# Performance work log

Measured on AMD Instinct MI355X. Metric: run time of the kernel, lower is better.

The kernel has to match this reference:

```python
import jax, jax.numpy as jnp
import numpy as np

VOCAB = 400000
DIM = 300
NUM_QUERIES = 512
TOP_K = 5


def setup_inputs() -> dict:
    key = jax.random.key(0)
    k1, k2 = jax.random.split(key)
    embedding = jax.random.normal(k1, (VOCAB, DIM), dtype=jnp.float32)
    word_ids = jax.random.randint(k2, (NUM_QUERIES,), 0, VOCAB, dtype=jnp.int64)
    return {"embedding": embedding, "word_ids": word_ids, "k": TOP_K}


def reference(embedding, word_ids, k):
    # Row-normalize the table (done in Synonym.__init__: emb / emb.norm(dim=1, keepdim=True))
    E = embedding / jnp.linalg.norm(embedding, axis=1, keepdims=True)  # [V, d]
    # Per-word GEMV against the full table, batched over queries:
    # torch.mm(word_embedding.view(1,-1), embedding.t()) per word -> [Q, V]
    q = E[word_ids]                      # [Q, d] gather of query word vectors
    sims = jnp.einsum('qd,vd->qv', q, E)  # [Q, V] cosine similarities
    # topk(k, largest=True); the torch code sorts results by value afterwards,
    # lax.top_k already returns values in descending order.
    top_vals, top_ids = jax.lax.top_k(sims, k)  # [Q, k], [Q, k]
    return top_vals, top_ids
```

## Files before the change

kernel.cpp:

```cpp
#include <hip/hip_runtime.h>


#define VOCAB   400000
#define DIM     300
#define NQ      512
#define NT      25000
#define TILE_U  5120
#define QFSTR   304
#define TOPK    5
#define NCAND   3072

using f32x4 = __attribute__((ext_vector_type(4))) float;
using s16x8 = __attribute__((ext_vector_type(8))) short;

__device__ __forceinline__ unsigned short f2bf(float f) {
  unsigned int u = __builtin_bit_cast(unsigned int, f);
  u += 0x7fffu + ((u >> 16) & 1u);
  return (unsigned short)(u >> 16);
}

__device__ __forceinline__ void ins3(float v, int id, float* tv, int* ti) {
  if (v > tv[2]) {
    if (v > tv[0]) {
      tv[2] = tv[1]; ti[2] = ti[1]; tv[1] = tv[0]; ti[1] = ti[0];
      tv[0] = v; ti[0] = id;
    } else if (v > tv[1]) {
      tv[2] = tv[1]; ti[2] = ti[1]; tv[1] = v; ti[1] = id;
    } else {
      tv[2] = v; ti[2] = id;
    }
  }
}

__global__ __launch_bounds__(64)
void qprep_kernel(const float* __restrict__ emb, const int* __restrict__ wid,
                  float* __restrict__ qf, unsigned short* __restrict__ qsw) {
  const int q = blockIdx.x;
  const int lane = threadIdx.x;
  const long long w = (long long)wid[q];
  const float* row = emb + w * DIM;
  float x[5];
  double ss = 0.0;
#pragma unroll
  for (int j = 0; j < 5; ++j) {
    const int k = lane + 64 * j;
    x[j] = (k < DIM) ? row[k] : 0.0f;
    ss += (double)x[j] * (double)x[j];
  }
#pragma unroll
  for (int m = 1; m < 64; m <<= 1) ss += __shfl_xor(ss, m, 64);
  const double rinv = 1.0 / sqrt(ss);
#pragma unroll
  for (int j = 0; j < 5; ++j) {
    const int k = lane + 64 * j;
    if (k < DIM) qf[q * QFSTR + k] = (float)((double)x[j] * rinv);
  }
  if (lane < 40) {
    const int ks = lane >> 2, grp = lane & 3;
    const int k0 = ks * 32 + grp * 8;
    unsigned int pw[4];
#pragma unroll
    for (int h = 0; h < 4; ++h) {
      const int k = k0 + 2 * h;
      float v0 = 0.f, v1 = 0.f;
      if (k < DIM)     v0 = (float)((double)row[k] * rinv);
      if (k + 1 < DIM) v1 = (float)((double)row[k + 1] * rinv);
      pw[h] = (unsigned int)f2bf(v0) | ((unsigned int)f2bf(v1) << 16);
    }
    uint4 pk; pk.x = pw[0]; pk.y = pw[1]; pk.z = pw[2]; pk.w = pw[3];
    *(uint4*)(qsw + (size_t)(q >> 4) * TILE_U + ks * 512 + grp * 128 + (q & 15) * 8) = pk;
  }
}

__global__ __launch_bounds__(256)
void prenorm_kernel(const float* __restrict__ emb, unsigned short* __restrict__ sw) {
  const int wave = threadIdx.x >> 6, lane = threadIdx.x & 63;
  const int t = blockIdx.x * 4 + wave;
  const int r = lane & 15, grp = lane >> 4;
  const float* row = emb + (size_t)(t * 16 + r) * DIM;

  float x[10][8];
  float ss = 0.f;
#pragma unroll
  for (int ks = 0; ks < 10; ++ks) {
    const int k0 = ks * 32 + grp * 8;
    if (k0 + 8 <= DIM) {
      const f32x4 u = *(const f32x4*)(row + k0);
      const f32x4 v = *(const f32x4*)(row + k0 + 4);
#pragma unroll
      for (int j = 0; j < 4; ++j) { x[ks][j] = u[j]; x[ks][j + 4] = v[j]; }
    } else {
#pragma unroll
      for (int j = 0; j < 8; ++j) {
        const int k = k0 + j;
        x[ks][j] = (k < DIM) ? row[k] : 0.0f;
      }
    }
#pragma unroll
    for (int j = 0; j < 8; ++j) ss += x[ks][j] * x[ks][j];
  }
  ss += __shfl_xor(ss, 16, 64);
  ss += __shfl_xor(ss, 32, 64);
  const float rinv = rsqrtf(ss);

  unsigned short* dst = sw + (size_t)t * TILE_U + lane * 8;
#pragma unroll
  for (int ks = 0; ks < 10; ++ks) {
    uint4 pk;
    unsigned int w0 = f2bf(x[ks][0] * rinv) | ((unsigned int)f2bf(x[ks][1] * rinv) << 16);
    unsigned int w1 = f2bf(x[ks][2] * rinv) | ((unsigned int)f2bf(x[ks][3] * rinv) << 16);
    unsigned int w2 = f2bf(x[ks][4] * rinv) | ((unsigned int)f2bf(x[ks][5] * rinv) << 16);
    unsigned int w3 = f2bf(x[ks][6] * rinv) | ((unsigned int)f2bf(x[ks][7] * rinv) << 16);
    pk.x = w0; pk.y = w1; pk.z = w2; pk.w = w3;
    *(uint4*)(dst + ks * 512) = pk;
  }
}

__global__ __launch_bounds__(256, 4)
void score_kernel(const unsigned short* __restrict__ sw,
                  const unsigned short* __restrict__ qsw,
                  float2* __restrict__ cand) {
  __shared__ __align__(16) unsigned short qlds[4 * TILE_U];

  const int tid = threadIdx.x;
  const int wave = tid >> 6, lane = tid & 63;
  const int l15 = lane & 15, grp = lane >> 4;
  const int bid = blockIdx.x;
  const int moct = (bid >> 3) & 7;
  const int rb = (bid & 7) | ((bid >> 6) << 3);

  {
    const uint4* src = (const uint4*)(qsw + (size_t)moct * 4 * TILE_U);
    uint4* dst = (uint4*)qlds;
#pragma unroll
    for (int i = 0; i < 10; ++i) dst[tid + 256 * i] = src[tid + 256 * i];
  }
  __syncthreads();

  float v3[4][3]; int i3[4][3];
#pragma unroll
  for (int qi = 0; qi < 4; ++qi)
#pragma unroll
    for (int j = 0; j < 3; ++j) { v3[qi][j] = -1e30f; i3[qi][j] = 0; }

  const unsigned short* bq = qlds + lane * 8;
  const int wt = rb * 16 + wave * 4;
  const int nit = (wt < 424) ? 13 : 12;

  for (int it = 0; it < nit; ++it) {
    const int t0 = it * 2048 + wt;
    const unsigned short* ap = sw + (size_t)t0 * TILE_U + lane * 8;

    f32x4 acc[4][4];
#pragma unroll
    for (int qi = 0; qi < 4; ++qi)
#pragma unroll
      for (int vi = 0; vi < 4; ++vi) acc[qi][vi] = {0.f, 0.f, 0.f, 0.f};

#pragma unroll
    for (int ks = 0; ks < 10; ++ks) {
      s16x8 a[4];
#pragma unroll
      for (int vi = 0; vi < 4; ++vi)
        a[vi] = *(const s16x8*)(ap + (size_t)vi * TILE_U + ks * 512);
#pragma unroll
      for (int qi = 0; qi < 4; ++qi) {
        const s16x8 b = *(const s16x8*)(bq + qi * TILE_U + ks * 512);
#pragma unroll
        for (int vi = 0; vi < 4; ++vi)
          acc[qi][vi] = __builtin_amdgcn_mfma_f32_16x16x32_bf16(a[vi], b, acc[qi][vi], 0, 0, 0);
      }
    }

#pragma unroll
    for (int vi = 0; vi < 4; ++vi) {
      const int rbase = (t0 + vi) * 16 + grp * 4;
#pragma unroll
      for (int qi = 0; qi < 4; ++qi) {
        const f32x4 a4 = acc[qi][vi];
        const float m01 = fmaxf(a4[0], a4[1]);
        const float m23 = fmaxf(a4[2], a4[3]);
        if (fmaxf(m01, m23) > v3[qi][2]) {
#pragma unroll
          for (int rr = 0; rr < 4; ++rr)
            ins3(a4[rr], rbase + rr, &v3[qi][0], &i3[qi][0]);
        }
      }
    }
  }

#pragma unroll
  for (int qi = 0; qi < 4; ++qi) {
    float m0 = v3[qi][0], m1 = v3[qi][1], m2 = v3[qi][2];
    int   d0 = i3[qi][0], d1 = i3[qi][1], d2 = i3[qi][2];
    const int q = moct * 64 + qi * 16 + l15;
    float2* dst = cand + (size_t)q * NCAND + (rb * 24 + wave * 6);
#pragma unroll
    for (int r = 0; r < 6; ++r) {
      float bv = m0; int bi = d0; int bl = grp;
      float ov = __shfl_xor(bv, 16, 64);
      int   oi = __shfl_xor(bi, 16, 64);
      int   ol = __shfl_xor(bl, 16, 64);
      if (ov > bv || (ov == bv && ol < bl)) { bv = ov; bi = oi; bl = ol; }
      ov = __shfl_xor(bv, 32, 64);
      oi = __shfl_xor(bi, 32, 64);
      ol = __shfl_xor(bl, 32, 64);
      if (ov > bv || (ov == bv && ol < bl)) { bv = ov; bi = oi; bl = ol; }
      if (bl == grp) { m0 = m1; d0 = d1; m1 = m2; d1 = d2; m2 = -1e30f; }
      if (r == grp || r == grp + 4) {
        float2 e; e.x = bv; e.y = __int_as_float(bi);
        dst[r] = e;
      }
    }
  }
}

__global__ __launch_bounds__(256)
void topk_kernel(const float* __restrict__ emb, const float* __restrict__ qf,
                 const float2* __restrict__ cand, float* __restrict__ out) {
  __shared__ float pV[256 * 6];
  __shared__ int   pI[256 * 6];
  __shared__ int   selI[32];
  __shared__ float resV[32];

  const int q = blockIdx.x;
  const int t = threadIdx.x;
  const float2* cq = cand + (size_t)q * NCAND;

  float bv[6]; int bi[6];
#pragma unroll
  for (int j = 0; j < 6; ++j) { bv[j] = -1e30f; bi[j] = -1; }
  for (int i = t; i < NCAND; i += 256) {
    const float2 e = cq[i];
    const float v = e.x;
    if (v > bv[5]) {
      bv[5] = v; bi[5] = __float_as_int(e.y);
#pragma unroll
      for (int j = 5; j > 0; --j) {
        if (bv[j] > bv[j - 1]) {
          const float tv2 = bv[j]; bv[j] = bv[j - 1]; bv[j - 1] = tv2;
          const int ti2 = bi[j]; bi[j] = bi[j - 1]; bi[j - 1] = ti2;
        }
      }
    }
  }
#pragma unroll
  for (int j = 0; j < 6; ++j) { pV[t * 6 + j] = bv[j]; pI[t * 6 + j] = bi[j]; }
  __syncthreads();

  if (t < 64) {
    for (int r = 0; r < 32; ++r) {
      float mv = -2e30f; int mp = 0;
      for (int i = t; i < 256 * 6; i += 64) {
        const float v = pV[i];
        if (v > mv) { mv = v; mp = i; }
      }
#pragma unroll
      for (int m = 1; m < 64; m <<= 1) {
        const float ov = __shfl_xor(mv, m, 64);
        const int   op = __shfl_xor(mp, m, 64);
        if (ov > mv) { mv = ov; mp = op; }
      }
      if (t == 0) { selI[r] = pI[mp]; pV[mp] = -2e30f; }
      __builtin_amdgcn_wave_barrier();
    }
  }
  __syncthreads();

  {
    const int j = t >> 3, sub = t & 7;
    const int id = selI[j];
    float dot = 0.f, sq = 0.f;
    if (id >= 0) {
      const f32x4* e4 = (const f32x4*)(emb + (size_t)id * DIM);
      const f32x4* q4 = (const f32x4*)(qf + (size_t)q * QFSTR);
      for (int f = sub; f < DIM / 4; f += 8) {
        const f32x4 ev = e4[f], qv = q4[f];
        dot += ev[0]*qv[0] + ev[1]*qv[1] + ev[2]*qv[2] + ev[3]*qv[3];
        sq  += ev[0]*ev[0] + ev[1]*ev[1] + ev[2]*ev[2] + ev[3]*ev[3];
      }
    }
#pragma unroll
    for (int m = 1; m < 8; m <<= 1) {
      dot += __shfl_xor(dot, m, 64);
      sq  += __shfl_xor(sq, m, 64);
    }
    if (sub == 0)
      resV[j] = (id >= 0 && sq > 0.f) ? (float)((double)dot / sqrt((double)sq)) : -2e30f;
  }
  __syncthreads();

  if (t == 0) {
#pragma unroll
    for (int r = 0; r < TOPK; ++r) {
      float mv = -3e30f; int mp = 0;
      for (int i = 0; i < 32; ++i) if (resV[i] > mv) { mv = resV[i]; mp = i; }
      out[q * TOPK + r] = mv;
      out[NQ * TOPK + q * TOPK + r] = (float)selI[mp];
      resV[mp] = -3e30f;
    }
  }
}

extern "C" void kernel_launch(void* const* d_in, const int* in_sizes, int n_in,
                              void* d_out, int out_size, void* d_ws, size_t ws_size,
                              hipStream_t stream) {
  (void)in_sizes; (void)n_in; (void)out_size; (void)ws_size;
  const float* emb = (const float*)d_in[0];
  const int* wid = (const int*)d_in[1];
  float* out = (float*)d_out;

  char* ws = (char*)d_ws;
  unsigned short* qsw = (unsigned short*)ws;
  float*  qf   = (float*)(ws + 327680);
  float2* cand = (float2*)(ws + 950272);
  unsigned short* sw = (unsigned short*)(ws + 13533184);

  qprep_kernel<<<NQ, 64, 0, stream>>>(emb, wid, qf, qsw);
  prenorm_kernel<<<NT / 4, 256, 0, stream>>>(emb, sw);
  score_kernel<<<1024, 256, 0, stream>>>(sw, qsw, cand);
  topk_kernel<<<NQ, 256, 0, stream>>>(emb, qf, cand, out);
}
```

Measured before the change: 1.246 ms.

## Restructure score kernel into 512-thread blocks with register double-buffered A loads

The score kernel now uses 512-thread blocks that each hold 128 queries in LDS. Each wave handles 2 vocab tiles by 64 queries rather than 4 by 64, and the next k-slice of the table is prefetched into registers (double-buffered) so global loads overlap the MFMAs. The prenorm kernel stages 64 rows into LDS with coalesced vector loads before normalizing, replacing the strided per-row reads. Together these aim to hide memory latency and cut uncoalesced traffic, at the cost of more LDS per block, which may lower occupancy.

```diff
diff --git a/kernel.cpp b/kernel.cpp
--- a/kernel.cpp
+++ b/kernel.cpp
@@ -74,10 +74,25 @@
 
 __global__ __launch_bounds__(256)
 void prenorm_kernel(const float* __restrict__ emb, unsigned short* __restrict__ sw) {
-  const int wave = threadIdx.x >> 6, lane = threadIdx.x & 63;
-  const int t = blockIdx.x * 4 + wave;
+  __shared__ __align__(16) float rows[64 * 300];
+
+  const int tid = threadIdx.x;
+  const int bid = blockIdx.x;
+  {
+    const f32x4* src = (const f32x4*)(emb + (size_t)bid * 64 * 300);
+    f32x4* dst = (f32x4*)rows;
+#pragma unroll
+    for (int i = 0; i < 19; ++i) {
+      const int idx = tid + 256 * i;
+      if (idx < 4800) dst[idx] = src[idx];
+    }
+  }
+  __syncthreads();
+
+  const int wave = tid >> 6, lane = tid & 63;
+  const int t = bid * 4 + wave;
   const int r = lane & 15, grp = lane >> 4;
-  const float* row = emb + (size_t)(t * 16 + r) * DIM;
+  const float* row = rows + (wave * 16 + r) * 300;
 
   float x[10][8];
   float ss = 0.f;
@@ -116,24 +131,26 @@
   }
 }
 
-__global__ __launch_bounds__(256, 4)
+__global__ __launch_bounds__(512, 4)
 void score_kernel(const unsigned short* __restrict__ sw,
                   const unsigned short* __restrict__ qsw,
                   float2* __restrict__ cand) {
-  __shared__ __align__(16) unsigned short qlds[4 * TILE_U];
+  __shared__ __align__(16) unsigned short qlds[8 * TILE_U];
 
   const int tid = threadIdx.x;
   const int wave = tid >> 6, lane = tid & 63;
   const int l15 = lane & 15, grp = lane >> 4;
   const int bid = blockIdx.x;
-  const int moct = (bid >> 3) & 7;
-  const int rb = (bid & 7) | ((bid >> 6) << 3);
+  const int rest = bid >> 3;
+  const int m = rest & 3;
+  const int s = (bid & 7) | ((rest >> 2) << 3);
+  const int wr = wave >> 1, qhalf = wave & 1;
 
   {
-    const uint4* src = (const uint4*)(qsw + (size_t)moct * 4 * TILE_U);
+    const uint4* src = (const uint4*)(qsw + (size_t)m * 8 * TILE_U);
     uint4* dst = (uint4*)qlds;
 #pragma unroll
-    for (int i = 0; i < 10; ++i) dst[tid + 256 * i] = src[tid + 256 * i];
+    for (int i = 0; i < 10; ++i) dst[tid + 512 * i] = src[tid + 512 * i];
   }
   __syncthreads();
 
@@ -143,37 +160,57 @@
 #pragma unroll
     for (int j = 0; j < 3; ++j) { v3[qi][j] = -1e30f; i3[qi][j] = 0; }
 
-  const unsigned short* bq = qlds + lane * 8;
-  const int wt = rb * 16 + wave * 4;
-  const int nit = (wt < 424) ? 13 : 12;
+  const unsigned short* aw = sw + lane * 8;
+  const unsigned short* bw = qlds + (size_t)qhalf * 4 * TILE_U + lane * 8;
+  const int wt = s * 8 + wr * 2;
+  const int nit = (s < 53) ? 25 : 24;
+
+  s16x8 ab[2][2];
+  {
+    const unsigned w0 = (unsigned)wt * TILE_U;
+    ab[0][0] = *(const s16x8*)(aw + w0);
+    ab[0][1] = *(const s16x8*)(aw + w0 + TILE_U);
+    ab[1][0] = *(const s16x8*)(aw + w0 + 512);
+    ab[1][1] = *(const s16x8*)(aw + w0 + TILE_U + 512);
+  }
 
   for (int it = 0; it < nit; ++it) {
-    const int t0 = it * 2048 + wt;
-    const unsigned short* ap = sw + (size_t)t0 * TILE_U + lane * 8;
-
-    f32x4 acc[4][4];
-#pragma unroll
-    for (int qi = 0; qi < 4; ++qi)
-#pragma unroll
-      for (int vi = 0; vi < 4; ++vi) acc[qi][vi] = {0.f, 0.f, 0.f, 0.f};
+    const int t0 = it * 1024 + wt;
+    const unsigned toff = (unsigned)t0 * TILE_U;
+
+    f32x4 acc[4][2];
+#pragma unroll
+    for (int qi = 0; qi < 4; ++qi) {
+      acc[qi][0] = {0.f, 0.f, 0.f, 0.f};
+      acc[qi][1] = {0.f, 0.f, 0.f, 0.f};
+    }
 
 #pragma unroll
     for (int ks = 0; ks < 10; ++ks) {
-      s16x8 a[4];
-#pragma unroll
-      for (int vi = 0; vi < 4; ++vi)
-        a[vi] = *(const s16x8*)(ap + (size_t)vi * TILE_U + ks * 512);
+      unsigned poff;
+      if (ks < 8) {
+        poff = toff + (unsigned)(ks + 2) * 512;
+      } else {
+        const unsigned ntoff =
+            (it + 1 < nit) ? toff + 1024u * TILE_U : (unsigned)wt * TILE_U;
+        poff = ntoff + (unsigned)(ks - 8) * 512;
+      }
+      const s16x8 p0 = *(const s16x8*)(aw + poff);
+      const s16x8 p1 = *(const s16x8*)(aw + poff + TILE_U);
+
+      const unsigned short* bb = bw + ks * 512;
 #pragma unroll
       for (int qi = 0; qi < 4; ++qi) {
-        const s16x8 b = *(const s16x8*)(bq + qi * TILE_U + ks * 512);
-#pragma unroll
-        for (int vi = 0; vi < 4; ++vi)
-          acc[qi][vi] = __builtin_amdgcn_mfma_f32_16x16x32_bf16(a[vi], b, acc[qi][vi], 0, 0, 0);
-      }
-    }
-
-#pragma unroll
-    for (int vi = 0; vi < 4; ++vi) {
+        const s16x8 b = *(const s16x8*)(bb + qi * TILE_U);
+        acc[qi][0] = __builtin_amdgcn_mfma_f32_16x16x32_bf16(ab[ks & 1][0], b, acc[qi][0], 0, 0, 0);
+        acc[qi][1] = __builtin_amdgcn_mfma_f32_16x16x32_bf16(ab[ks & 1][1], b, acc[qi][1], 0, 0, 0);
+      }
+      ab[ks & 1][0] = p0;
+      ab[ks & 1][1] = p1;
+    }
+
+#pragma unroll
+    for (int vi = 0; vi < 2; ++vi) {
       const int rbase = (t0 + vi) * 16 + grp * 4;
 #pragma unroll
       for (int qi = 0; qi < 4; ++qi) {
@@ -193,8 +230,8 @@
   for (int qi = 0; qi < 4; ++qi) {
     float m0 = v3[qi][0], m1 = v3[qi][1], m2 = v3[qi][2];
     int   d0 = i3[qi][0], d1 = i3[qi][1], d2 = i3[qi][2];
-    const int q = moct * 64 + qi * 16 + l15;
-    float2* dst = cand + (size_t)q * NCAND + (rb * 24 + wave * 6);
+    const int q = m * 128 + qhalf * 64 + qi * 16 + l15;
+    float2* dst = cand + (size_t)q * NCAND + ((s * 4 + wr) * 6);
 #pragma unroll
     for (int r = 0; r < 6; ++r) {
       float bv = m0; int bi = d0; int bl = grp;
@@ -317,7 +354,7 @@
   unsigned short* sw = (unsigned short*)(ws + 13533184);
 
   qprep_kernel<<<NQ, 64, 0, stream>>>(emb, wid, qf, qsw);
-  prenorm_kernel<<<NT / 4, 256, 0, stream>>>(emb, sw);
-  score_kernel<<<1024, 256, 0, stream>>>(sw, qsw, cand);
+  prenorm_kernel<<<VOCAB / 64, 256, 0, stream>>>(emb, sw);
+  score_kernel<<<512, 512, 0, stream>>>(sw, qsw, cand);
   topk_kernel<<<NQ, 256, 0, stream>>>(emb, qf, cand, out);
 }
```

Result: slower. 1.293 ms (+3.8%).
